# Optimization experiments

Measured on AMD Instinct MI355X. Metric: run time of the kernel, lower is better.

Reference implementation:

```python
import jax, jax.numpy as jnp
import numpy as np

N_NODES = 50000
N_EDGES = 800000
D = 128


def gcn_conv(x, src, dst, W, b, n):
    # PyG GCNConv: h = x @ W; add self-loops; symmetric normalization
    # D^{-1/2} (A + I) D^{-1/2}; aggregate at destination; add bias.
    loop = jnp.arange(n, dtype=src.dtype)
    s = jnp.concatenate([src, loop])
    d = jnp.concatenate([dst, loop])
    deg = jax.ops.segment_sum(jnp.ones_like(d, dtype=x.dtype), d, num_segments=n)
    dinv = jnp.where(deg > 0, jax.lax.rsqrt(deg), 0.0)
    norm = dinv[s] * dinv[d]  # [E+N]
    h = x @ W                  # [N, hidden]
    msg = norm[:, None] * h[s]  # gather -> [E+N, hidden]
    out = jax.ops.segment_sum(msg, d, num_segments=n)  # scatter-add
    return out + b


def setup_inputs() -> dict:
    key = jax.random.key(0)
    ks = jax.random.split(key, 6)
    x = jax.random.normal(ks[0], (N_NODES, D), dtype=jnp.float32)
    edge_index = jax.random.randint(ks[1], (2, N_EDGES), 0, N_NODES, dtype=jnp.int32)
    sc = 1.0 / np.sqrt(D)
    W1 = jax.random.normal(ks[2], (D, D), dtype=jnp.float32) * sc
    b1 = jnp.zeros((D,), dtype=jnp.float32)
    W2 = jax.random.normal(ks[3], (D, D), dtype=jnp.float32) * sc
    b2 = jnp.zeros((D,), dtype=jnp.float32)
    lin_W = jax.random.normal(ks[4], (2 * D, D), dtype=jnp.float32) * (1.0 / np.sqrt(2 * D))
    lin_b = jnp.zeros((D,), dtype=jnp.float32)
    return {"x": x, "edge_index": edge_index, "W1": W1, "b1": b1,
            "W2": W2, "b2": b2, "lin_W": lin_W, "lin_b": lin_b}


def reference(x, edge_index, W1, b1, W2, b2, lin_W, lin_b):
    n = x.shape[0]
    src, dst = edge_index[0], edge_index[1]
    x1 = jax.nn.relu(gcn_conv(x, src, dst, W1, b1, n))
    x2 = jax.nn.relu(gcn_conv(x1, src, dst, W2, b2, n))
    jk = jnp.concatenate([x1, x2], axis=-1)  # JumpingKnowledge 'cat'
    return jk @ lin_W + lin_b
```

## Files before the change

kernel.cpp:

```cpp
#include <hip/hip_runtime.h>


#define D128 128

typedef __attribute__((ext_vector_type(8))) short bf16x8;
typedef __attribute__((ext_vector_type(4))) float f32x4;

__device__ __forceinline__ unsigned short f2bf_bits(float v) {
    unsigned int u = __float_as_uint(v);
    unsigned int r = u + 0x7FFFu + ((u >> 16) & 1u);
    return (unsigned short)(r >> 16);
}
__device__ __forceinline__ float bf2f(unsigned short h) {
    return __uint_as_float(((unsigned int)h) << 16);
}

__global__ void k_count(const int* __restrict__ dst, int* __restrict__ indeg, int E) {
    int e = blockIdx.x * 256 + threadIdx.x;
    if (e < E) atomicAdd(&indeg[dst[e]], 1);
}

__global__ void k_scan1(const int* __restrict__ indeg, int* __restrict__ row_ptr,
                        int* __restrict__ bsum, float* __restrict__ dinv, int n) {
    __shared__ int tmp[256];
    int i = blockIdx.x * 256 + threadIdx.x;
    int v = (i < n) ? indeg[i] : 0;
    if (i < n) dinv[i] = rsqrtf((float)(v + 1));
    tmp[threadIdx.x] = v;
    __syncthreads();
    for (int off = 1; off < 256; off <<= 1) {
        int t = (threadIdx.x >= off) ? tmp[threadIdx.x - off] : 0;
        __syncthreads();
        tmp[threadIdx.x] += t;
        __syncthreads();
    }
    if (i < n) row_ptr[i] = tmp[threadIdx.x] - v;
    if (threadIdx.x == 255) bsum[blockIdx.x] = tmp[255];
}

__global__ void k_scan2(int* __restrict__ bsum, int nb) {
    __shared__ int tmp[256];
    int v = (threadIdx.x < nb) ? bsum[threadIdx.x] : 0;
    tmp[threadIdx.x] = v;
    __syncthreads();
    for (int off = 1; off < 256; off <<= 1) {
        int t = (threadIdx.x >= off) ? tmp[threadIdx.x - off] : 0;
        __syncthreads();
        tmp[threadIdx.x] += t;
        __syncthreads();
    }
    if (threadIdx.x < nb) bsum[threadIdx.x] = tmp[threadIdx.x] - v;
}

__global__ void k_scan3(int* __restrict__ row_ptr, const int* __restrict__ bsum,
                        int* __restrict__ cursor, int n, int E) {
    int i = blockIdx.x * 256 + threadIdx.x;
    if (i < n) {
        int r = row_ptr[i] + bsum[blockIdx.x];
        row_ptr[i] = r;
        cursor[i] = r;
    }
    if (blockIdx.x == 0 && threadIdx.x == 0) row_ptr[n] = E;
}

__global__ void k_fill(const int* __restrict__ src, const int* __restrict__ dst,
                       const float* __restrict__ dinv, int* __restrict__ cursor,
                       float2* __restrict__ csr, int E) {
    int e = blockIdx.x * 256 + threadIdx.x;
    if (e >= E) return;
    int s = src[e], d = dst[e];
    int pos = atomicAdd(&cursor[d], 1);
    csr[pos] = make_float2(__int_as_float(s), dinv[s] * dinv[d]);
}

__global__ __launch_bounds__(256) void k_agg_csr(
    const unsigned int* __restrict__ h, const int* __restrict__ row_ptr,
    const float2* __restrict__ csr, const float* __restrict__ dinv,
    const float* __restrict__ bias, float* __restrict__ o, int n)
{
    int node = blockIdx.x * 4 + (threadIdx.x >> 6);
    int lane = threadIdx.x & 63;
    if (node >= n) return;
    float dv = dinv[node];
    unsigned int su = h[node * 64 + lane];
    float ax = dv * dv * __uint_as_float(su << 16);
    float ay = dv * dv * __uint_as_float(su & 0xFFFF0000u);
    int j = row_ptr[node], end = row_ptr[node + 1];
    for (; j + 7 < end; j += 8) {
        float2 c0 = csr[j+0], c1 = csr[j+1], c2 = csr[j+2], c3 = csr[j+3];
        float2 c4 = csr[j+4], c5 = csr[j+5], c6 = csr[j+6], c7 = csr[j+7];
        unsigned int u0 = h[__float_as_int(c0.x) * 64 + lane];
        unsigned int u1 = h[__float_as_int(c1.x) * 64 + lane];
        unsigned int u2 = h[__float_as_int(c2.x) * 64 + lane];
        unsigned int u3 = h[__float_as_int(c3.x) * 64 + lane];
        unsigned int u4 = h[__float_as_int(c4.x) * 64 + lane];
        unsigned int u5 = h[__float_as_int(c5.x) * 64 + lane];
        unsigned int u6 = h[__float_as_int(c6.x) * 64 + lane];
        unsigned int u7 = h[__float_as_int(c7.x) * 64 + lane];
        ax += c0.y*__uint_as_float(u0 << 16) + c1.y*__uint_as_float(u1 << 16)
            + c2.y*__uint_as_float(u2 << 16) + c3.y*__uint_as_float(u3 << 16)
            + c4.y*__uint_as_float(u4 << 16) + c5.y*__uint_as_float(u5 << 16)
            + c6.y*__uint_as_float(u6 << 16) + c7.y*__uint_as_float(u7 << 16);
        ay += c0.y*__uint_as_float(u0 & 0xFFFF0000u) + c1.y*__uint_as_float(u1 & 0xFFFF0000u)
            + c2.y*__uint_as_float(u2 & 0xFFFF0000u) + c3.y*__uint_as_float(u3 & 0xFFFF0000u)
            + c4.y*__uint_as_float(u4 & 0xFFFF0000u) + c5.y*__uint_as_float(u5 & 0xFFFF0000u)
            + c6.y*__uint_as_float(u6 & 0xFFFF0000u) + c7.y*__uint_as_float(u7 & 0xFFFF0000u);
    }
    for (; j + 3 < end; j += 4) {
        float2 c0 = csr[j+0], c1 = csr[j+1], c2 = csr[j+2], c3 = csr[j+3];
        unsigned int u0 = h[__float_as_int(c0.x) * 64 + lane];
        unsigned int u1 = h[__float_as_int(c1.x) * 64 + lane];
        unsigned int u2 = h[__float_as_int(c2.x) * 64 + lane];
        unsigned int u3 = h[__float_as_int(c3.x) * 64 + lane];
        ax += c0.y*__uint_as_float(u0 << 16) + c1.y*__uint_as_float(u1 << 16)
            + c2.y*__uint_as_float(u2 << 16) + c3.y*__uint_as_float(u3 << 16);
        ay += c0.y*__uint_as_float(u0 & 0xFFFF0000u) + c1.y*__uint_as_float(u1 & 0xFFFF0000u)
            + c2.y*__uint_as_float(u2 & 0xFFFF0000u) + c3.y*__uint_as_float(u3 & 0xFFFF0000u);
    }
    for (; j < end; ++j) {
        float2 c = csr[j];
        unsigned int u = h[__float_as_int(c.x) * 64 + lane];
        ax += c.y * __uint_as_float(u << 16);
        ay += c.y * __uint_as_float(u & 0xFFFF0000u);
    }
    float2 bv = ((const float2*)bias)[lane];
    float2 ov = {fmaxf(ax + bv.x, 0.f), fmaxf(ay + bv.y, 0.f)};
    ((float2*)o)[node * 64 + lane] = ov;
}

__global__ __launch_bounds__(256, 2) void k_gemm_mfma(
    const float* __restrict__ A0, const float* __restrict__ A1,
    const float* __restrict__ W, const float* __restrict__ bias,
    float* __restrict__ C, int n, int nhalf, int out_bf)
{
    __shared__ unsigned short Ah[4 * 4 * 64 * 8];
    __shared__ unsigned short Al[4 * 4 * 64 * 8];
    int tid = threadIdx.x;
    int l = tid & 63;
    int wv = tid >> 6;
    int brow = blockIdx.x * 64;
    int colbase = wv * 32;
    int lanen = l & 15;
    int kb = (l >> 4) * 8;

    f32x4 acc[4][2];
#pragma unroll
    for (int m = 0; m < 4; ++m)
#pragma unroll
        for (int t = 0; t < 2; ++t) acc[m][t] = (f32x4){0.f, 0.f, 0.f, 0.f};

    for (int h = 0; h < nhalf; ++h) {
        if (h) __syncthreads();
        const float* A = (h == 0) ? A0 : A1;

        const float4* A4 = (const float4*)(A + (size_t)brow * D128);
#pragma unroll
        for (int it = 0; it < 8; ++it) {
            int f = it * 256 + tid;
            int r = f >> 5, k4 = f & 31;
            float4 v = make_float4(0.f, 0.f, 0.f, 0.f);
            if (brow + r < n) v = A4[f];
            int lane_ = (r & 15) + 16 * ((k4 >> 1) & 3);
            int base = ((((k4 >> 3) * 4 + (r >> 4)) * 64 + lane_) << 3) + (k4 & 1) * 4;
            float vv[4] = {v.x, v.y, v.z, v.w};
            ushort4 hh, ll;
            unsigned short* hp = (unsigned short*)&hh;
            unsigned short* lp = (unsigned short*)&ll;
#pragma unroll
            for (int q = 0; q < 4; ++q) {
                unsigned short hb = f2bf_bits(vv[q]);
                hp[q] = hb;
                lp[q] = f2bf_bits(vv[q] - bf2f(hb));
            }
            *(ushort4*)&Ah[base] = hh;
            *(ushort4*)&Al[base] = ll;
        }
        __syncthreads();

        bf16x8 wh[2][4], wl[2][4];
        const float* Wh = W + (size_t)h * 128 * D128;
#pragma unroll
        for (int t = 0; t < 2; ++t)
#pragma unroll
            for (int s = 0; s < 4; ++s) {
#pragma unroll
                for (int j = 0; j < 8; ++j) {
                    float v = Wh[(size_t)(s * 32 + kb + j) * D128 + colbase + t * 16 + lanen];
                    unsigned short hb = f2bf_bits(v);
                    wh[t][s][j] = (short)hb;
                    wl[t][s][j] = (short)f2bf_bits(v - bf2f(hb));
                }
            }

#pragma unroll
        for (int s = 0; s < 4; ++s) {
#pragma unroll
            for (int m = 0; m < 4; ++m) {
                int fb = ((s * 4 + m) * 64 + l) * 8;
                bf16x8 ah = *(const bf16x8*)&Ah[fb];
                bf16x8 al = *(const bf16x8*)&Al[fb];
#pragma unroll
                for (int t = 0; t < 2; ++t) {
                    acc[m][t] = __builtin_amdgcn_mfma_f32_16x16x32_bf16(ah, wh[t][s], acc[m][t], 0, 0, 0);
                    acc[m][t] = __builtin_amdgcn_mfma_f32_16x16x32_bf16(al, wh[t][s], acc[m][t], 0, 0, 0);
                    acc[m][t] = __builtin_amdgcn_mfma_f32_16x16x32_bf16(ah, wl[t][s], acc[m][t], 0, 0, 0);
                }
            }
        }
    }

    float bv[2] = {0.f, 0.f};
    if (bias) { bv[0] = bias[colbase + lanen]; bv[1] = bias[colbase + 16 + lanen]; }
    int rsub = (l >> 4) * 4;
    if (out_bf) {
        unsigned short* Cb = (unsigned short*)C;
#pragma unroll
        for (int m = 0; m < 4; ++m)
#pragma unroll
            for (int t = 0; t < 2; ++t)
#pragma unroll
                for (int r = 0; r < 4; ++r) {
                    int row = brow + m * 16 + rsub + r;
                    if (row < n)
                        Cb[(size_t)row * D128 + colbase + t * 16 + lanen] = f2bf_bits(acc[m][t][r]);
                }
    } else {
#pragma unroll
        for (int m = 0; m < 4; ++m)
#pragma unroll
            for (int t = 0; t < 2; ++t)
#pragma unroll
                for (int r = 0; r < 4; ++r) {
                    int row = brow + m * 16 + rsub + r;
                    if (row < n)
                        C[(size_t)row * D128 + colbase + t * 16 + lanen] = acc[m][t][r] + bv[t];
                }
    }
}

extern "C" void kernel_launch(void* const* d_in, const int* in_sizes, int n_in,
                              void* d_out, int out_size, void* d_ws, size_t ws_size,
                              hipStream_t stream) {
    const float* x    = (const float*)d_in[0];
    const int*   ei   = (const int*)d_in[1];
    const float* W1   = (const float*)d_in[2];
    const float* b1   = (const float*)d_in[3];
    const float* W2   = (const float*)d_in[4];
    const float* b2   = (const float*)d_in[5];
    const float* linW = (const float*)d_in[6];
    const float* linb = (const float*)d_in[7];

    int n = in_sizes[0] / D128;
    int E = in_sizes[1] / 2;
    const int* src = ei;
    const int* dst = ei + E;

    float* out = (float*)d_out;
    float* ws  = (float*)d_ws;

    size_t o = 0;
    float2* csr   = (float2*)(ws + o);  o += 2 * (size_t)E;
    int*   indeg  = (int*)(ws + o);     o += n;
    float* dinv   = ws + o;             o += n;
    int*   row_ptr= (int*)(ws + o);     o += n + 1;
    int*   bsum   = (int*)(ws + o);     o += 256;
    int*   cursor = (int*)(ws + o);     o += n;
    o = (o + 3) & ~(size_t)3;
    float* x1     = ws + o;             o += (size_t)n * D128;
    float* x2     = ws + o;
    float* h      = out;

    int gn = (n + 255) / 256;
    int gE = (E + 255) / 256;
    int gemmBlocks = (n + 63) / 64;
    int aggBlocks  = (n + 3) / 4;

    (void)hipMemsetAsync(indeg, 0, (size_t)n * sizeof(int), stream);
    k_count<<<gE, 256, 0, stream>>>(dst, indeg, E);
    k_scan1<<<gn, 256, 0, stream>>>(indeg, row_ptr, bsum, dinv, n);
    k_scan2<<<1, 256, 0, stream>>>(bsum, gn);
    k_scan3<<<gn, 256, 0, stream>>>(row_ptr, bsum, cursor, n, E);
    k_fill<<<gE, 256, 0, stream>>>(src, dst, dinv, cursor, csr, E);

    k_gemm_mfma<<<gemmBlocks, 256, 0, stream>>>(x, nullptr, W1, nullptr, h, n, 1, 1);
    k_agg_csr<<<aggBlocks, 256, 0, stream>>>((const unsigned int*)h, row_ptr, csr, dinv, b1, x1, n);

    k_gemm_mfma<<<gemmBlocks, 256, 0, stream>>>(x1, nullptr, W2, nullptr, h, n, 1, 1);
    k_agg_csr<<<aggBlocks, 256, 0, stream>>>((const unsigned int*)h, row_ptr, csr, dinv, b2, x2, n);

    k_gemm_mfma<<<gemmBlocks, 256, 0, stream>>>(x1, x2, linW, linb, out, n, 2, 0);
}
```

Measured before the change: 254.7 us.

## Fuse CSR fill into first GEMM and share x1 across dual GEMM

The CSR fill kernel is merged into the first GEMM launch as extra blocks, so both run concurrently in one grid. The second-layer GEMM now also computes x1 @ linW[:128] in the same pass, reusing the staged x1 tile, and the final GEMM only multiplies x2 by the bottom half of linW and accumulates into out. This removes a kernel launch and a second read and split of x1, at the cost of higher register pressure in the dual GEMM and a read-modify-write of out. The bf16 h buffer moves from the output to workspace.

```diff
diff --git a/kernel.cpp b/kernel.cpp
--- a/kernel.cpp
+++ b/kernel.cpp
@@ -13,6 +13,12 @@
 }
 __device__ __forceinline__ float bf2f(unsigned short h) {
     return __uint_as_float(((unsigned int)h) << 16);
+}
+__device__ __forceinline__ void mfma3(f32x4& acc, bf16x8 ah, bf16x8 al,
+                                      bf16x8 wh, bf16x8 wl) {
+    acc = __builtin_amdgcn_mfma_f32_16x16x32_bf16(ah, wh, acc, 0, 0, 0);
+    acc = __builtin_amdgcn_mfma_f32_16x16x32_bf16(al, wh, acc, 0, 0, 0);
+    acc = __builtin_amdgcn_mfma_f32_16x16x32_bf16(ah, wl, acc, 0, 0, 0);
 }
 
 __global__ void k_count(const int* __restrict__ dst, int* __restrict__ indeg, int E) {
@@ -61,16 +67,6 @@
         cursor[i] = r;
     }
     if (blockIdx.x == 0 && threadIdx.x == 0) row_ptr[n] = E;
-}
-
-__global__ void k_fill(const int* __restrict__ src, const int* __restrict__ dst,
-                       const float* __restrict__ dinv, int* __restrict__ cursor,
-                       float2* __restrict__ csr, int E) {
-    int e = blockIdx.x * 256 + threadIdx.x;
-    if (e >= E) return;
-    int s = src[e], d = dst[e];
-    int pos = atomicAdd(&cursor[d], 1);
-    csr[pos] = make_float2(__int_as_float(s), dinv[s] * dinv[d]);
 }
 
 __global__ __launch_bounds__(256) void k_agg_csr(
@@ -128,10 +124,158 @@
     ((float2*)o)[node * 64 + lane] = ov;
 }
 
+__device__ __forceinline__ void stage_A_tile(
+    const float* __restrict__ A, int brow, int n, int tid,
+    unsigned short* __restrict__ Ah, unsigned short* __restrict__ Al)
+{
+    const float4* A4 = (const float4*)(A + (size_t)brow * D128);
+#pragma unroll
+    for (int it = 0; it < 8; ++it) {
+        int f = it * 256 + tid;
+        int r = f >> 5, k4 = f & 31;
+        float4 v = make_float4(0.f, 0.f, 0.f, 0.f);
+        if (brow + r < n) v = A4[f];
+        int lane_ = (r & 15) + 16 * ((k4 >> 1) & 3);
+        int base = ((((k4 >> 3) * 4 + (r >> 4)) * 64 + lane_) << 3) + (k4 & 1) * 4;
+        float vv[4] = {v.x, v.y, v.z, v.w};
+        ushort4 hh, ll;
+        unsigned short* hp = (unsigned short*)&hh;
+        unsigned short* lp = (unsigned short*)&ll;
+#pragma unroll
+        for (int q = 0; q < 4; ++q) {
+            unsigned short hb = f2bf_bits(vv[q]);
+            hp[q] = hb;
+            lp[q] = f2bf_bits(vv[q] - bf2f(hb));
+        }
+        *(ushort4*)&Ah[base] = hh;
+        *(ushort4*)&Al[base] = ll;
+    }
+}
+
+__device__ __forceinline__ void load_W_s(
+    const float* __restrict__ W, int s, int colbase, int lanen, int kb,
+    bf16x8 wh[2], bf16x8 wl[2])
+{
+#pragma unroll
+    for (int t = 0; t < 2; ++t)
+#pragma unroll
+        for (int j = 0; j < 8; ++j) {
+            float v = W[(size_t)(s * 32 + kb + j) * D128 + colbase + t * 16 + lanen];
+            unsigned short hb = f2bf_bits(v);
+            wh[t][j] = (short)hb;
+            wl[t][j] = (short)f2bf_bits(v - bf2f(hb));
+        }
+}
+
+__device__ __forceinline__ void epilogue(
+    f32x4 acc[4][2], float* __restrict__ C, const float* __restrict__ bias,
+    int brow, int n, int colbase, int lanen, int l, int out_bf, int addC)
+{
+    float bv[2] = {0.f, 0.f};
+    if (bias) { bv[0] = bias[colbase + lanen]; bv[1] = bias[colbase + 16 + lanen]; }
+    int rsub = (l >> 4) * 4;
+    if (out_bf) {
+        unsigned short* Cb = (unsigned short*)C;
+#pragma unroll
+        for (int m = 0; m < 4; ++m)
+#pragma unroll
+            for (int t = 0; t < 2; ++t)
+#pragma unroll
+                for (int r = 0; r < 4; ++r) {
+                    int row = brow + m * 16 + rsub + r;
+                    if (row < n)
+                        Cb[(size_t)row * D128 + colbase + t * 16 + lanen] = f2bf_bits(acc[m][t][r]);
+                }
+    } else {
+#pragma unroll
+        for (int m = 0; m < 4; ++m)
+#pragma unroll
+            for (int t = 0; t < 2; ++t)
+#pragma unroll
+                for (int r = 0; r < 4; ++r) {
+                    int row = brow + m * 16 + rsub + r;
+                    if (row < n) {
+                        size_t idx = (size_t)row * D128 + colbase + t * 16 + lanen;
+                        float v = acc[m][t][r] + bv[t];
+                        if (addC) v += C[idx];
+                        C[idx] = v;
+                    }
+                }
+    }
+}
+
+__device__ __forceinline__ void gemm_core(
+    const float* __restrict__ A, const float* __restrict__ W,
+    const float* __restrict__ bias, float* __restrict__ C,
+    int n, int out_bf, int addC, int bid, int tid,
+    unsigned short* __restrict__ Ah, unsigned short* __restrict__ Al)
+{
+    int l = tid & 63;
+    int wv = tid >> 6;
+    int brow = bid * 64;
+    int colbase = wv * 32;
+    int lanen = l & 15;
+    int kb = (l >> 4) * 8;
+
+    f32x4 acc[4][2];
+#pragma unroll
+    for (int m = 0; m < 4; ++m)
+#pragma unroll
+        for (int t = 0; t < 2; ++t) acc[m][t] = (f32x4){0.f, 0.f, 0.f, 0.f};
+
+    stage_A_tile(A, brow, n, tid, Ah, Al);
+    __syncthreads();
+
+#pragma unroll
+    for (int s = 0; s < 4; ++s) {
+        bf16x8 wh[2], wl[2];
+        load_W_s(W, s, colbase, lanen, kb, wh, wl);
+#pragma unroll
+        for (int m = 0; m < 4; ++m) {
+            int fb = ((s * 4 + m) * 64 + l) * 8;
+            bf16x8 ah = *(const bf16x8*)&Ah[fb];
+            bf16x8 al = *(const bf16x8*)&Al[fb];
+#pragma unroll
+            for (int t = 0; t < 2; ++t) mfma3(acc[m][t], ah, al, wh[t], wl[t]);
+        }
+    }
+    epilogue(acc, C, bias, brow, n, colbase, lanen, l, out_bf, addC);
+}
+
+__global__ __launch_bounds__(256, 2) void k_gemm1_fill(
+    const float* __restrict__ x, const float* __restrict__ W1,
+    float* __restrict__ h, int n,
+    const int* __restrict__ src, const int* __restrict__ dst,
+    const float* __restrict__ dinv, int* __restrict__ cursor,
+    float2* __restrict__ csr, int E, int gemmBlocks)
+{
+    __shared__ unsigned short Ah[4 * 4 * 64 * 8];
+    __shared__ unsigned short Al[4 * 4 * 64 * 8];
+    if (blockIdx.x < gemmBlocks) {
+        gemm_core(x, W1, nullptr, h, n, 1, 0, blockIdx.x, threadIdx.x, Ah, Al);
+    } else {
+        int e = (blockIdx.x - gemmBlocks) * 256 + threadIdx.x;
+        if (e >= E) return;
+        int s = src[e], d = dst[e];
+        int pos = atomicAdd(&cursor[d], 1);
+        csr[pos] = make_float2(__int_as_float(s), dinv[s] * dinv[d]);
+    }
+}
+
 __global__ __launch_bounds__(256, 2) void k_gemm_mfma(
-    const float* __restrict__ A0, const float* __restrict__ A1,
-    const float* __restrict__ W, const float* __restrict__ bias,
-    float* __restrict__ C, int n, int nhalf, int out_bf)
+    const float* __restrict__ A, const float* __restrict__ W,
+    const float* __restrict__ bias, float* __restrict__ C,
+    int n, int out_bf, int addC)
+{
+    __shared__ unsigned short Ah[4 * 4 * 64 * 8];
+    __shared__ unsigned short Al[4 * 4 * 64 * 8];
+    gemm_core(A, W, bias, C, n, out_bf, addC, blockIdx.x, threadIdx.x, Ah, Al);
+}
+
+__global__ __launch_bounds__(256, 2) void k_gemm_dual(
+    const float* __restrict__ A, const float* __restrict__ W2,
+    const float* __restrict__ Wtop, float* __restrict__ hOut,
+    float* __restrict__ pOut, int n)
 {
     __shared__ unsigned short Ah[4 * 4 * 64 * 8];
     __shared__ unsigned short Al[4 * 4 * 64 * 8];
@@ -143,99 +287,37 @@
     int lanen = l & 15;
     int kb = (l >> 4) * 8;
 
-    f32x4 acc[4][2];
+    f32x4 accA[4][2], accB[4][2];
 #pragma unroll
     for (int m = 0; m < 4; ++m)
 #pragma unroll
-        for (int t = 0; t < 2; ++t) acc[m][t] = (f32x4){0.f, 0.f, 0.f, 0.f};
-
-    for (int h = 0; h < nhalf; ++h) {
-        if (h) __syncthreads();
-        const float* A = (h == 0) ? A0 : A1;
-
-        const float4* A4 = (const float4*)(A + (size_t)brow * D128);
-#pragma unroll
-        for (int it = 0; it < 8; ++it) {
-            int f = it * 256 + tid;
-            int r = f >> 5, k4 = f & 31;
-            float4 v = make_float4(0.f, 0.f, 0.f, 0.f);
-            if (brow + r < n) v = A4[f];
-            int lane_ = (r & 15) + 16 * ((k4 >> 1) & 3);
-            int base = ((((k4 >> 3) * 4 + (r >> 4)) * 64 + lane_) << 3) + (k4 & 1) * 4;
-            float vv[4] = {v.x, v.y, v.z, v.w};
-            ushort4 hh, ll;
-            unsigned short* hp = (unsigned short*)&hh;
-            unsigned short* lp = (unsigned short*)&ll;
-#pragma unroll
-            for (int q = 0; q < 4; ++q) {
-                unsigned short hb = f2bf_bits(vv[q]);
-                hp[q] = hb;
-                lp[q] = f2bf_bits(vv[q] - bf2f(hb));
+        for (int t = 0; t < 2; ++t) {
+            accA[m][t] = (f32x4){0.f, 0.f, 0.f, 0.f};
+            accB[m][t] = (f32x4){0.f, 0.f, 0.f, 0.f};
+        }
+
+    stage_A_tile(A, brow, n, tid, Ah, Al);
+    __syncthreads();
+
+#pragma unroll
+    for (int s = 0; s < 4; ++s) {
+        bf16x8 whA[2], wlA[2], whB[2], wlB[2];
+        load_W_s(W2, s, colbase, lanen, kb, whA, wlA);
+        load_W_s(Wtop, s, colbase, lanen, kb, whB, wlB);
+#pragma unroll
+        for (int m = 0; m < 4; ++m) {
+            int fb = ((s * 4 + m) * 64 + l) * 8;
+            bf16x8 ah = *(const bf16x8*)&Ah[fb];
+            bf16x8 al = *(const bf16x8*)&Al[fb];
+#pragma unroll
+            for (int t = 0; t < 2; ++t) {
+                mfma3(accA[m][t], ah, al, whA[t], wlA[t]);
+                mfma3(accB[m][t], ah, al, whB[t], wlB[t]);
             }
-            *(ushort4*)&Ah[base] = hh;
-            *(ushort4*)&Al[base] = ll;
-        }
-        __syncthreads();
-
-        bf16x8 wh[2][4], wl[2][4];
-        const float* Wh = W + (size_t)h * 128 * D128;
-#pragma unroll
-        for (int t = 0; t < 2; ++t)
-#pragma unroll
-            for (int s = 0; s < 4; ++s) {
-#pragma unroll
-                for (int j = 0; j < 8; ++j) {
-                    float v = Wh[(size_t)(s * 32 + kb + j) * D128 + colbase + t * 16 + lanen];
-                    unsigned short hb = f2bf_bits(v);
-                    wh[t][s][j] = (short)hb;
-                    wl[t][s][j] = (short)f2bf_bits(v - bf2f(hb));
-                }
-            }
-
-#pragma unroll
-        for (int s = 0; s < 4; ++s) {
-#pragma unroll
-            for (int m = 0; m < 4; ++m) {
-                int fb = ((s * 4 + m) * 64 + l) * 8;
-                bf16x8 ah = *(const bf16x8*)&Ah[fb];
-                bf16x8 al = *(const bf16x8*)&Al[fb];
-#pragma unroll
-                for (int t = 0; t < 2; ++t) {
-                    acc[m][t] = __builtin_amdgcn_mfma_f32_16x16x32_bf16(ah, wh[t][s], acc[m][t], 0, 0, 0);
-                    acc[m][t] = __builtin_amdgcn_mfma_f32_16x16x32_bf16(al, wh[t][s], acc[m][t], 0, 0, 0);
-                    acc[m][t] = __builtin_amdgcn_mfma_f32_16x16x32_bf16(ah, wl[t][s], acc[m][t], 0, 0, 0);
-                }
-            }
-        }
-    }
-
-    float bv[2] = {0.f, 0.f};
-    if (bias) { bv[0] = bias[colbase + lanen]; bv[1] = bias[colbase + 16 + lanen]; }
-    int rsub = (l >> 4) * 4;
-    if (out_bf) {
-        unsigned short* Cb = (unsigned short*)C;
-#pragma unroll
-        for (int m = 0; m < 4; ++m)
-#pragma unroll
-            for (int t = 0; t < 2; ++t)
-#pragma unroll
-                for (int r = 0; r < 4; ++r) {
-                    int row = brow + m * 16 + rsub + r;
-                    if (row < n)
-                        Cb[(size_t)row * D128 + colbase + t * 16 + lanen] = f2bf_bits(acc[m][t][r]);
-                }
-    } else {
-#pragma unroll
-        for (int m = 0; m < 4; ++m)
-#pragma unroll
-            for (int t = 0; t < 2; ++t)
-#pragma unroll
-                for (int r = 0; r < 4; ++r) {
-                    int row = brow + m * 16 + rsub + r;
-                    if (row < n)
-                        C[(size_t)row * D128 + colbase + t * 16 + lanen] = acc[m][t][r] + bv[t];
-                }
-    }
+        }
+    }
+    epilogue(accA, hOut, nullptr, brow, n, colbase, lanen, l, 1, 0);
+    epilogue(accB, pOut, nullptr, brow, n, colbase, lanen, l, 0, 0);
 }
 
 extern "C" void kernel_launch(void* const* d_in, const int* in_sizes, int n_in,
@@ -267,8 +349,8 @@
     int*   cursor = (int*)(ws + o);     o += n;
     o = (o + 3) & ~(size_t)3;
     float* x1     = ws + o;             o += (size_t)n * D128;
-    float* x2     = ws + o;
-    float* h      = out;
+    float* x2     = ws + o;             o += (size_t)n * D128;
+    float* h      = ws + o;
 
     int gn = (n + 255) / 256;
     int gE = (E + 255) / 256;
@@ -280,13 +362,15 @@
     k_scan1<<<gn, 256, 0, stream>>>(indeg, row_ptr, bsum, dinv, n);
     k_scan2<<<1, 256, 0, stream>>>(bsum, gn);
     k_scan3<<<gn, 256, 0, stream>>>(row_ptr, bsum, cursor, n, E);
-    k_fill<<<gE, 256, 0, stream>>>(src, dst, dinv, cursor, csr, E);
-
-    k_gemm_mfma<<<gemmBlocks, 256, 0, stream>>>(x, nullptr, W1, nullptr, h, n, 1, 1);
+
+    k_gemm1_fill<<<gemmBlocks + gE, 256, 0, stream>>>(
+        x, W1, h, n, src, dst, dinv, cursor, csr, E, gemmBlocks);
+
     k_agg_csr<<<aggBlocks, 256, 0, stream>>>((const unsigned int*)h, row_ptr, csr, dinv, b1, x1, n);
 
-    k_gemm_mfma<<<gemmBlocks, 256, 0, stream>>>(x1, nullptr, W2, nullptr, h, n, 1, 1);
+    k_gemm_dual<<<gemmBlocks, 256, 0, stream>>>(x1, W2, linW, h, out, n);
+
     k_agg_csr<<<aggBlocks, 256, 0, stream>>>((const unsigned int*)h, row_ptr, csr, dinv, b2, x2, n);
 
-    k_gemm_mfma<<<gemmBlocks, 256, 0, stream>>>(x1, x2, linW, linb, out, n, 2, 0);
-}
+    k_gemm_mfma<<<gemmBlocks, 256, 0, stream>>>(x2, linW + 128 * D128, linb, out, n, 0, 1);
+}
```

New measurement: 228.5 us. 10.3% less time.
